# Performance work log

Hardware: AMD Instinct MI355X
Metric: run time of the kernel (lower is better)

## Reference

```python
import jax, jax.numpy as jnp
import numpy as np

K = 3
STRIDE = 1
PAD = 1
C_IN = 128
C_OUT = 256

def setup_inputs() -> dict:
    key = jax.random.key(0)
    kx, kw, kb = jax.random.split(key, 3)
    x = jax.random.normal(kx, (32, C_IN, 56, 56), dtype=jnp.float32)
    # torch init: uniform(-1/K, 1/K) for kernels, uniform(-1/sqrt(Cout), 1/sqrt(Cout)) for bias
    kernels = jax.random.uniform(kw, (C_OUT, C_IN, K, K), dtype=jnp.float32,
                                 minval=-1.0 / K, maxval=1.0 / K)
    b = jax.random.uniform(kb, (C_OUT,), dtype=jnp.float32,
                           minval=-1.0 / C_OUT ** 0.5, maxval=1.0 / C_OUT ** 0.5)
    return {"x": x, "kernels": kernels, "b": b}

def reference(x, kernels, b):
    # Same math as the im2col broadcast-matmul + channel-sum: a standard 2D conv
    # with zero padding, expressed as one contracted GEMM via conv_general_dilated.
    out = jax.lax.conv_general_dilated(
        x, kernels,
        window_strides=(STRIDE, STRIDE),
        padding=((PAD, PAD), (PAD, PAD)),
        dimension_numbers=("NCHW", "OIHW", "NCHW"),
    )
    return out + b.reshape(1, C_OUT, 1, 1)
```

## Files before the change

### kernel.cpp

```cpp
#include <hip/hip_runtime.h>
#include <hip/hip_bf16.h>

#define NB   32
#define CIN  128
#define COUT 256
#define HH   56
#define WW   56
#define CH   59

typedef __attribute__((ext_vector_type(8))) short short8;
typedef __attribute__((ext_vector_type(4))) float f32x4;

__device__ __forceinline__ unsigned short f2bf(float f) {
    unsigned int u = __builtin_bit_cast(unsigned int, f);
    u = u + 0x7fffu + ((u >> 16) & 1u);
    return (unsigned short)(u >> 16);
}

__device__ __forceinline__ void glds16(const unsigned short* g, unsigned short* l) {
    __builtin_amdgcn_global_load_lds(
        (const __attribute__((address_space(1))) unsigned int*)g,
        (__attribute__((address_space(3))) unsigned int*)l,
        16, 0, 0);
}

__global__ __launch_bounds__(256) void wpose_kernel(const float* __restrict__ w,
                                                    unsigned short* __restrict__ wt2) {
    int q = blockIdx.x * 256 + threadIdx.x;
    if (q >= 36 * 16 * 64 * 8) return;
    int j = q & 7;
    int l = (q >> 3) & 63;
    int f = (q >> 9) & 15;
    int s = q >> 13;
    int g = l >> 4, r = l & 15;
    int t = s >> 2, cc = s & 3;
    int o = f * 16 + r;
    int c = cc * 32 + g * 8 + j;
    wt2[q] = f2bf(w[((size_t)o * CIN + c) * 9 + t]);
}

__global__ __launch_bounds__(512, 2) void conv_mfma_kernel(
        const float* __restrict__ x,
        const unsigned short* __restrict__ wt2,
        const float* __restrict__ bias,
        float* __restrict__ out) {
    __shared__ unsigned short ldsB[6 * 16 * CH * 8];
    __shared__ unsigned short ldsA[8 * 2 * 2048];

    const int tid  = threadIdx.x;
    const int h0   = blockIdx.x * 4, n = blockIdx.y;
    const int wid  = tid >> 6, lane = tid & 63;
    const int wm   = wid >> 1, wn = wid & 1;
    const int g    = lane >> 4, r = lane & 15;

    for (int i = tid; i < 6 * 16 * CH; i += 512) {
        uint4 z = {0u, 0u, 0u, 0u};
        *(uint4*)&ldsB[(size_t)i * 8] = z;
    }
    __syncthreads();

    {
        const float* xn = x + (size_t)n * CIN * HH * WW;
        for (int i = tid; i < 6 * 64 * 14; i += 512) {
            int w4  = i % 14;
            int t1  = i / 14;
            int cp  = t1 & 63;
            int row = t1 >> 6;
            int hs  = h0 + row - 1;
            if ((unsigned)hs < HH) {
                const float* p = xn + ((size_t)(2 * cp) * HH + hs) * WW + 4 * w4;
                float4 va = *(const float4*)p;
                float4 vb = *(const float4*)(p + HH * WW);
                int gc = cp >> 2, e = cp & 3;
                #pragma unroll
                for (int j = 0; j < 4; ++j) {
                    int wpos = 4 * w4 + j + 1;
                    unsigned int pk = (unsigned int)f2bf(((const float*)&va)[j])
                                    | ((unsigned int)f2bf(((const float*)&vb)[j]) << 16);
                    ((unsigned int*)ldsB)[((row * 16 + gc) * CH + wpos) * 4 + e] = pk;
                }
            }
        }
    }

    unsigned short* aslot = &ldsA[(size_t)wid * 2 * 2048];
    #define STAGE_A(slot, s)                                                    \
        {                                                                       \
            const unsigned short* asrc_ =                                       \
                wt2 + ((size_t)(s) * 16 + wm * 4) * 512 + lane * 8;             \
            unsigned short* adst_ = aslot + (slot) * 2048;                      \
            glds16(asrc_,        adst_);                                        \
            glds16(asrc_ + 512,  adst_ + 512);                                  \
            glds16(asrc_ + 1024, adst_ + 1024);                                 \
            glds16(asrc_ + 1536, adst_ + 1536);                                 \
        }

    STAGE_A(0, 0);
    __syncthreads();

    const unsigned short* bbase[7];
    #pragma unroll
    for (int ni = 0; ni < 7; ++ni) {
        int c  = ni * 16 + r;
        int hr = (c >= 56) ? 1 : 0;
        int lo = hr * (16 * CH) + (c - hr * 56);
        bbase[ni] = &ldsB[(size_t)((wn * 32 + g) * CH + lo) * 8];
    }

    f32x4 acc[4][7];
    #pragma unroll
    for (int mi = 0; mi < 4; ++mi)
        #pragma unroll
        for (int ni = 0; ni < 7; ++ni)
            #pragma unroll
            for (int v = 0; v < 4; ++v) acc[mi][ni][v] = 0.f;

    const unsigned short* aread = aslot + lane * 8;

    #pragma unroll
    for (int t = 0; t < 9; ++t) {
        const int kh = t / 3, kw = t - 3 * (t / 3);
        #pragma unroll
        for (int cc = 0; cc < 4; ++cc) {
            const int s = t * 4 + cc;
            const int p = s & 1;
            const int boff = kh * 15104 + cc * 3776 + kw * 16;

            if (s < 35) STAGE_A(p ^ 1, s + 1);

            if (s < 35) asm volatile("s_waitcnt vmcnt(4)" ::: "memory");
            else        asm volatile("s_waitcnt vmcnt(0)" ::: "memory");

            short8 a[4];
            #pragma unroll
            for (int mi = 0; mi < 4; ++mi)
                a[mi] = *(const short8*)(aread + p * 2048 + mi * 512);

            short8 b[7];
            #pragma unroll
            for (int ni = 0; ni < 7; ++ni)
                b[ni] = *(const short8*)((const char*)bbase[ni] + boff);

            #pragma unroll
            for (int mi = 0; mi < 4; ++mi)
                #pragma unroll
                for (int ni = 0; ni < 7; ++ni)
                    acc[mi][ni] = __builtin_amdgcn_mfma_f32_16x16x32_bf16(
                        a[mi], b[ni], acc[mi][ni], 0, 0, 0);
        }
    }

    #pragma unroll
    for (int mi = 0; mi < 4; ++mi) {
        const int o0 = wm * 64 + mi * 16 + 4 * g;
        const float4 bv = *(const float4*)&bias[o0];
        #pragma unroll
        for (int ni = 0; ni < 7; ++ni) {
            const int c  = ni * 16 + r;
            const int hr = (c >= 56) ? 1 : 0;
            const int h  = h0 + wn * 2 + hr;
            const int w  = c - hr * 56;
            #pragma unroll
            for (int v = 0; v < 4; ++v) {
                out[((size_t)(n * COUT + o0 + v) * HH + h) * WW + w] =
                    acc[mi][ni][v] + ((const float*)&bv)[v];
            }
        }
    }
}

extern "C" void kernel_launch(void* const* d_in, const int* in_sizes, int n_in,
                              void* d_out, int out_size, void* d_ws, size_t ws_size,
                              hipStream_t stream) {
    const float* x  = (const float*)d_in[0];
    const float* wk = (const float*)d_in[1];
    const float* b  = (const float*)d_in[2];
    float* out = (float*)d_out;

    unsigned short* wt2 = (unsigned short*)d_ws;

    wpose_kernel<<<(36 * 16 * 64 * 8 + 255) / 256, 256, 0, stream>>>(wk, wt2);
    dim3 gc(14, NB);
    conv_mfma_kernel<<<gc, 512, 0, stream>>>(x, wt2, b, out);
    (void)ws_size; (void)in_sizes; (void)n_in; (void)out_size;
}
```

Baseline: 73.44 us.

## Load weights directly from global, zero only halo LDS, overlap last input rows

The change drops the per-warp LDS double buffer for weight tiles filled by global_load_lds and instead reads the A fragments straight from global memory (L2/cache) each step. Only the padding columns and boundary rows of the input tile are zeroed now, not the whole tile. The input load is split so the first four rows are staged, then the first kernel row (kh=0) of MFMAs runs while the last two rows are still being loaded. The launch_bounds occupancy hint of 2 is removed. The cost is direct global-load latency on the weight fragments with no explicit prefetch, and it relies on the compiler and cache to hide it.

New measurement: 75.32 us. 1.03x slower.

```diff
diff --git a/kernel.cpp b/kernel.cpp
--- a/kernel.cpp
+++ b/kernel.cpp
@@ -17,13 +17,6 @@
     return (unsigned short)(u >> 16);
 }
 
-__device__ __forceinline__ void glds16(const unsigned short* g, unsigned short* l) {
-    __builtin_amdgcn_global_load_lds(
-        (const __attribute__((address_space(1))) unsigned int*)g,
-        (__attribute__((address_space(3))) unsigned int*)l,
-        16, 0, 0);
-}
-
 __global__ __launch_bounds__(256) void wpose_kernel(const float* __restrict__ w,
                                                     unsigned short* __restrict__ wt2) {
     int q = blockIdx.x * 256 + threadIdx.x;
@@ -39,13 +32,12 @@
     wt2[q] = f2bf(w[((size_t)o * CIN + c) * 9 + t]);
 }
 
-__global__ __launch_bounds__(512, 2) void conv_mfma_kernel(
+__global__ __launch_bounds__(512) void conv_mfma_kernel(
         const float* __restrict__ x,
         const unsigned short* __restrict__ wt2,
         const float* __restrict__ bias,
         float* __restrict__ out) {
     __shared__ unsigned short ldsB[6 * 16 * CH * 8];
-    __shared__ unsigned short ldsA[8 * 2 * 2048];
 
     const int tid  = threadIdx.x;
     const int h0   = blockIdx.x * 4, n = blockIdx.y;
@@ -53,50 +45,66 @@
     const int wm   = wid >> 1, wn = wid & 1;
     const int g    = lane >> 4, r = lane & 15;
 
-    for (int i = tid; i < 6 * 16 * CH; i += 512) {
-        uint4 z = {0u, 0u, 0u, 0u};
-        *(uint4*)&ldsB[(size_t)i * 8] = z;
+    const uint4 z = {0u, 0u, 0u, 0u};
+
+    if (tid < 192) {
+        int row = tid / 32, sub = tid & 31;
+        int gc = sub >> 1, wp = (sub & 1) ? 57 : 0;
+        *(uint4*)&ldsB[(size_t)((row * 16 + gc) * CH + wp) * 8] = z;
+    }
+    if (h0 == 0) {
+        for (int i = tid; i < 16 * CH; i += 512)
+            *(uint4*)&ldsB[(size_t)i * 8] = z;
+    }
+    if (h0 == 52) {
+        for (int i = tid; i < 16 * CH; i += 512)
+            *(uint4*)&ldsB[(size_t)(5 * 16 * CH + i) * 8] = z;
+    }
+
+    const float* xn = x + (size_t)n * CIN * HH * WW;
+
+    for (int i = tid; i < 4 * 64 * 14; i += 512) {
+        int w4  = i % 14;
+        int t1  = i / 14;
+        int cp  = t1 & 63;
+        int row = t1 >> 6;
+        int hs  = h0 + row - 1;
+        if ((unsigned)hs < HH) {
+            const float* p = xn + ((size_t)(2 * cp) * HH + hs) * WW + 4 * w4;
+            float4 va = *(const float4*)p;
+            float4 vb = *(const float4*)(p + HH * WW);
+            int gc = cp >> 2, e = cp & 3;
+            #pragma unroll
+            for (int j = 0; j < 4; ++j) {
+                int wpos = 4 * w4 + j + 1;
+                unsigned int pk = (unsigned int)f2bf(((const float*)&va)[j])
+                                | ((unsigned int)f2bf(((const float*)&vb)[j]) << 16);
+                ((unsigned int*)ldsB)[((row * 16 + gc) * CH + wpos) * 4 + e] = pk;
+            }
+        }
     }
     __syncthreads();
 
-    {
-        const float* xn = x + (size_t)n * CIN * HH * WW;
-        for (int i = tid; i < 6 * 64 * 14; i += 512) {
-            int w4  = i % 14;
-            int t1  = i / 14;
-            int cp  = t1 & 63;
-            int row = t1 >> 6;
-            int hs  = h0 + row - 1;
-            if ((unsigned)hs < HH) {
-                const float* p = xn + ((size_t)(2 * cp) * HH + hs) * WW + 4 * w4;
-                float4 va = *(const float4*)p;
-                float4 vb = *(const float4*)(p + HH * WW);
-                int gc = cp >> 2, e = cp & 3;
-                #pragma unroll
-                for (int j = 0; j < 4; ++j) {
-                    int wpos = 4 * w4 + j + 1;
-                    unsigned int pk = (unsigned int)f2bf(((const float*)&va)[j])
-                                    | ((unsigned int)f2bf(((const float*)&vb)[j]) << 16);
-                    ((unsigned int*)ldsB)[((row * 16 + gc) * CH + wpos) * 4 + e] = pk;
-                }
+    for (int i = tid; i < 2 * 64 * 14; i += 512) {
+        int w4  = i % 14;
+        int t1  = i / 14;
+        int cp  = t1 & 63;
+        int row = 4 + (t1 >> 6);
+        int hs  = h0 + row - 1;
+        if ((unsigned)hs < HH) {
+            const float* p = xn + ((size_t)(2 * cp) * HH + hs) * WW + 4 * w4;
+            float4 va = *(const float4*)p;
+            float4 vb = *(const float4*)(p + HH * WW);
+            int gc = cp >> 2, e = cp & 3;
+            #pragma unroll
+            for (int j = 0; j < 4; ++j) {
+                int wpos = 4 * w4 + j + 1;
+                unsigned int pk = (unsigned int)f2bf(((const float*)&va)[j])
+                                | ((unsigned int)f2bf(((const float*)&vb)[j]) << 16);
+                ((unsigned int*)ldsB)[((row * 16 + gc) * CH + wpos) * 4 + e] = pk;
             }
         }
     }
-
-    unsigned short* aslot = &ldsA[(size_t)wid * 2 * 2048];
-    #define STAGE_A(slot, s)                                                    \
-        {                                                                       \
-            const unsigned short* asrc_ =                                       \
-                wt2 + ((size_t)(s) * 16 + wm * 4) * 512 + lane * 8;             \
-            unsigned short* adst_ = aslot + (slot) * 2048;                      \
-            glds16(asrc_,        adst_);                                        \
-            glds16(asrc_ + 512,  adst_ + 512);                                  \
-            glds16(asrc_ + 1024, adst_ + 1024);                                 \
-            glds16(asrc_ + 1536, adst_ + 1536);                                 \
-        }
-
-    STAGE_A(0, 0);
-    __syncthreads();
 
     const unsigned short* bbase[7];
     #pragma unroll
@@ -115,40 +123,42 @@
             #pragma unroll
             for (int v = 0; v < 4; ++v) acc[mi][ni][v] = 0.f;
 
-    const unsigned short* aread = aslot + lane * 8;
+    const short8* abase = (const short8*)wt2 + (size_t)(wm * 4) * 64 + lane;
+
+    #define K_STEP(t_, cc_)                                                     \
+        {                                                                       \
+            const int s_ = (t_) * 4 + (cc_);                                    \
+            const int kh_ = (t_) / 3, kw_ = (t_) - 3 * ((t_) / 3);              \
+            const int boff_ = kh_ * 15104 + (cc_) * 3776 + kw_ * 16;            \
+            short8 a_[4];                                                       \
+            _Pragma("unroll")                                                   \
+            for (int mi = 0; mi < 4; ++mi)                                      \
+                a_[mi] = abase[(size_t)s_ * 1024 + mi * 64];                    \
+            short8 b_[7];                                                       \
+            _Pragma("unroll")                                                   \
+            for (int ni = 0; ni < 7; ++ni)                                      \
+                b_[ni] = *(const short8*)((const char*)bbase[ni] + boff_);      \
+            _Pragma("unroll")                                                   \
+            for (int mi = 0; mi < 4; ++mi)                                      \
+                _Pragma("unroll")                                               \
+                for (int ni = 0; ni < 7; ++ni)                                  \
+                    acc[mi][ni] = __builtin_amdgcn_mfma_f32_16x16x32_bf16(      \
+                        a_[mi], b_[ni], acc[mi][ni], 0, 0, 0);                  \
+        }
 
     #pragma unroll
-    for (int t = 0; t < 9; ++t) {
-        const int kh = t / 3, kw = t - 3 * (t / 3);
+    for (int t = 0; t < 3; ++t)
         #pragma unroll
-        for (int cc = 0; cc < 4; ++cc) {
-            const int s = t * 4 + cc;
-            const int p = s & 1;
-            const int boff = kh * 15104 + cc * 3776 + kw * 16;
+        for (int cc = 0; cc < 4; ++cc)
+            K_STEP(t, cc)
 
-            if (s < 35) STAGE_A(p ^ 1, s + 1);
+    __syncthreads();
 
-            if (s < 35) asm volatile("s_waitcnt vmcnt(4)" ::: "memory");
-            else        asm volatile("s_waitcnt vmcnt(0)" ::: "memory");
-
-            short8 a[4];
-            #pragma unroll
-            for (int mi = 0; mi < 4; ++mi)
-                a[mi] = *(const short8*)(aread + p * 2048 + mi * 512);
-
-            short8 b[7];
-            #pragma unroll
-            for (int ni = 0; ni < 7; ++ni)
-                b[ni] = *(const short8*)((const char*)bbase[ni] + boff);
-
-            #pragma unroll
-            for (int mi = 0; mi < 4; ++mi)
-                #pragma unroll
-                for (int ni = 0; ni < 7; ++ni)
-                    acc[mi][ni] = __builtin_amdgcn_mfma_f32_16x16x32_bf16(
-                        a[mi], b[ni], acc[mi][ni], 0, 0, 0);
-        }
-    }
+    #pragma unroll
+    for (int t = 3; t < 9; ++t)
+        #pragma unroll
+        for (int cc = 0; cc < 4; ++cc)
+            K_STEP(t, cc)
 
     #pragma unroll
     for (int mi = 0; mi < 4; ++mi) {
```

## Load weight fragments directly from global and zero only LDS halo regions

Applied to the files above, without the earlier changes.

Removes the per-wave double-buffered LDS staging of weight tiles (global_load_lds plus manual vmcnt waits) and reads A fragments straight from global memory into registers, relying on the compiler to schedule loads. It also drops the full LDS clear and its barrier, zeroing only the left/right padding columns and the top/bottom halo rows at image edges. The launch bound no longer requests two blocks per CU, and freeing the A staging buffer shrinks LDS use. The risk is exposed global-load latency in the MFMA loop, since prefetching is no longer explicit.

After: 78.94 us. 1.07x slower.

```diff
diff --git a/kernel.cpp b/kernel.cpp
--- a/kernel.cpp
+++ b/kernel.cpp
@@ -17,13 +17,6 @@
     return (unsigned short)(u >> 16);
 }
 
-__device__ __forceinline__ void glds16(const unsigned short* g, unsigned short* l) {
-    __builtin_amdgcn_global_load_lds(
-        (const __attribute__((address_space(1))) unsigned int*)g,
-        (__attribute__((address_space(3))) unsigned int*)l,
-        16, 0, 0);
-}
-
 __global__ __launch_bounds__(256) void wpose_kernel(const float* __restrict__ w,
                                                     unsigned short* __restrict__ wt2) {
     int q = blockIdx.x * 256 + threadIdx.x;
@@ -39,13 +32,12 @@
     wt2[q] = f2bf(w[((size_t)o * CIN + c) * 9 + t]);
 }
 
-__global__ __launch_bounds__(512, 2) void conv_mfma_kernel(
+__global__ __launch_bounds__(512) void conv_mfma_kernel(
         const float* __restrict__ x,
         const unsigned short* __restrict__ wt2,
         const float* __restrict__ bias,
         float* __restrict__ out) {
     __shared__ unsigned short ldsB[6 * 16 * CH * 8];
-    __shared__ unsigned short ldsA[8 * 2 * 2048];
 
     const int tid  = threadIdx.x;
     const int h0   = blockIdx.x * 4, n = blockIdx.y;
@@ -53,11 +45,22 @@
     const int wm   = wid >> 1, wn = wid & 1;
     const int g    = lane >> 4, r = lane & 15;
 
-    for (int i = tid; i < 6 * 16 * CH; i += 512) {
-        uint4 z = {0u, 0u, 0u, 0u};
-        *(uint4*)&ldsB[(size_t)i * 8] = z;
+    const uint4 z = {0u, 0u, 0u, 0u};
+
+    if (tid < 288) {
+        int row = tid / 48, sub = tid % 48;
+        int gc = sub / 3, k3 = sub % 3;
+        int wp = (k3 == 0) ? 0 : (56 + k3);
+        *(uint4*)&ldsB[(size_t)((row * 16 + gc) * CH + wp) * 8] = z;
     }
-    __syncthreads();
+    if (h0 == 0) {
+        for (int i = tid; i < 16 * CH; i += 512)
+            *(uint4*)&ldsB[(size_t)i * 8] = z;
+    }
+    if (h0 == 52) {
+        for (int i = tid; i < 16 * CH; i += 512)
+            *(uint4*)&ldsB[(size_t)(5 * 16 * CH + i) * 8] = z;
+    }
 
     {
         const float* xn = x + (size_t)n * CIN * HH * WW;
@@ -82,20 +85,6 @@
             }
         }
     }
-
-    unsigned short* aslot = &ldsA[(size_t)wid * 2 * 2048];
-    #define STAGE_A(slot, s)                                                    \
-        {                                                                       \
-            const unsigned short* asrc_ =                                       \
-                wt2 + ((size_t)(s) * 16 + wm * 4) * 512 + lane * 8;             \
-            unsigned short* adst_ = aslot + (slot) * 2048;                      \
-            glds16(asrc_,        adst_);                                        \
-            glds16(asrc_ + 512,  adst_ + 512);                                  \
-            glds16(asrc_ + 1024, adst_ + 1024);                                 \
-            glds16(asrc_ + 1536, adst_ + 1536);                                 \
-        }
-
-    STAGE_A(0, 0);
     __syncthreads();
 
     const unsigned short* bbase[7];
@@ -115,7 +104,7 @@
             #pragma unroll
             for (int v = 0; v < 4; ++v) acc[mi][ni][v] = 0.f;
 
-    const unsigned short* aread = aslot + lane * 8;
+    const short8* abase = (const short8*)wt2 + (size_t)(wm * 4) * 64 + lane;
 
     #pragma unroll
     for (int t = 0; t < 9; ++t) {
@@ -123,18 +112,12 @@
         #pragma unroll
         for (int cc = 0; cc < 4; ++cc) {
             const int s = t * 4 + cc;
-            const int p = s & 1;
             const int boff = kh * 15104 + cc * 3776 + kw * 16;
-
-            if (s < 35) STAGE_A(p ^ 1, s + 1);
-
-            if (s < 35) asm volatile("s_waitcnt vmcnt(4)" ::: "memory");
-            else        asm volatile("s_waitcnt vmcnt(0)" ::: "memory");
 
             short8 a[4];
             #pragma unroll
             for (int mi = 0; mi < 4; ++mi)
-                a[mi] = *(const short8*)(aread + p * 2048 + mi * 512);
+                a[mi] = abase[(size_t)s * 1024 + mi * 64];
 
             short8 b[7];
             #pragma unroll
```
